# Performance work log

Hardware: AMD Instinct MI355X
Metric: run time of the kernel (lower is better)

## Reference

```python
import jax, jax.numpy as jnp
import numpy as np

B, N, D = 256, 100000, 512
A, C, K = 256, 100, 32
EPS = 1e-8  # torch cosine_similarity eps


def setup_inputs() -> dict:
    key = jax.random.key(0)
    ks = jax.random.split(key, 10)
    s = lambda fan_in: 1.0 / np.sqrt(fan_in)
    return {
        "query_feat": jax.random.normal(ks[0], (B, D), jnp.float32),
        "memory_keys": jax.random.normal(ks[1], (N, D), jnp.float32),
        # query_dense: Linear(D, A)
        "Wq": jax.random.uniform(ks[2], (D, A), jnp.float32, -s(D), s(D)),
        "bq": jax.random.uniform(ks[3], (A,), jnp.float32, -s(D), s(D)),
        # memory_dense: Linear(D, A)
        "Wm": jax.random.uniform(ks[4], (D, A), jnp.float32, -s(D), s(D)),
        "bm": jax.random.uniform(ks[5], (A,), jnp.float32, -s(D), s(D)),
        # attention_score_dense: Linear(A, 1)
        "Ws": jax.random.uniform(ks[6], (A, 1), jnp.float32, -s(A), s(A)),
        "bs": jax.random.uniform(ks[7], (1,), jnp.float32, -s(A), s(A)),
        # classification_layer: Linear(2*D, C)
        "Wc": jax.random.uniform(ks[8], (2 * D, C), jnp.float32, -s(2 * D), s(2 * D)),
        "bc": jax.random.uniform(ks[9], (C,), jnp.float32, -s(2 * D), s(2 * D)),
    }


def reference(query_feat, memory_keys, Wq, bq, Wm, bm, Ws, bs, Wc, bc):
    # query embedding (visual encoder output) + relu
    q = jax.nn.relu(query_feat)  # [B, D]
    # ---- knn_search: cosine similarity + topk + gather ----
    qn = jnp.linalg.norm(q, axis=-1)            # [B]
    kn = jnp.linalg.norm(memory_keys, axis=-1)  # [N]
    sim = (q @ memory_keys.T) / jnp.maximum(qn[:, None] * kn[None, :], EPS)  # [B, N]
    _, idx = jax.lax.top_k(sim, K)              # [B, K]
    knn = memory_keys[idx]                      # [B, K, D]
    # ---- MemoryAttentionModule ----
    # tanh(query_dense(q)[:,None,:] + memory_dense(knn)) -> score -> softmax over K
    h = jnp.tanh((q @ Wq + bq)[:, None, :] + knn @ Wm + bm)  # [B, K, A]
    scores = h @ Ws + bs                                      # [B, K, 1]
    w = jax.nn.softmax(scores, axis=1)                        # [B, K, 1]
    attended = jnp.sum(w * knn, axis=1)                       # [B, D]
    # ---- classification ----
    merged = jnp.concatenate([q, attended], axis=1)           # [B, 2D]
    return merged @ Wc + bc                                   # [B, C]
```

## Files before the change

kernel.cpp:

```cpp
#include <hip/hip_runtime.h>
#include <hip/hip_bf16.h>
#include <hip/hip_fp16.h>

#define BQ    256
#define NKEY  100000
#define DD    512
#define AD    256
#define CD    100
#define KSEL  32
#define KB    64
#define NB    1563
#define CPQ   (NB*12)

#define NPART 8
#define WTOP  12
#define NC2   (NPART*4*WTOP)
#define TLA   6

typedef __attribute__((ext_vector_type(8))) short  short8_t;
typedef __attribute__((ext_vector_type(8))) __bf16 bf16x8;
typedef __attribute__((ext_vector_type(4))) float  f32x4;

__device__ __forceinline__ unsigned short f2bf(float x) {
  unsigned int u = __float_as_uint(x);
  return (unsigned short)((u + 0x7FFFu + ((u >> 16) & 1u)) >> 16);
}
__device__ __forceinline__ unsigned short f2bf_n(float x) {
  __bf16 h = (__bf16)x;
  return __builtin_bit_cast(unsigned short, h);
}
__device__ __forceinline__ float bf2f(unsigned short h) {
  return __uint_as_float(((unsigned int)h) << 16);
}
__device__ __forceinline__ f32x4 mfma_bf16(short8_t a, short8_t b, f32x4 c) {
  return __builtin_amdgcn_mfma_f32_16x16x32_bf16(
      __builtin_bit_cast(bf16x8, a), __builtin_bit_cast(bf16x8, b), c, 0, 0, 0);
}
__device__ __forceinline__ float fast_tanh(float x) {
  x = fminf(fmaxf(x, -15.f), 15.f);
  float e = __expf(2.f * x);
  return (e - 1.f) * __builtin_amdgcn_rcpf(e + 1.f);
}
__device__ __forceinline__ void gload_lds16(const float* g, float* l) {
  __builtin_amdgcn_global_load_lds((const __attribute__((address_space(1))) void*)g,
                                   (__attribute__((address_space(3))) void*)l, 16, 0, 0);
}

template<int T>
__device__ __forceinline__ void topk_insert(float (&v)[T], int (&ix)[T], float val, int idx) {
  if (val <= v[T-1]) return;
  v[T-1] = val; ix[T-1] = idx;
  #pragma unroll
  for (int j = T-1; j > 0; --j) {
    bool sw = v[j] > v[j-1];
    float tv = sw ? v[j] : v[j-1];  float uv = sw ? v[j-1] : v[j];
    int   ti = sw ? ix[j] : ix[j-1]; int  ui = sw ? ix[j-1] : ix[j];
    v[j-1] = tv; v[j] = uv; ix[j-1] = ti; ix[j] = ui;
  }
}

__global__ __launch_bounds__(256) void k0_prep(const float* __restrict__ qfeat,
                                               float* __restrict__ qr,
                                               unsigned short* __restrict__ qf,
                                               float* __restrict__ qn) {
  int b = blockIdx.x, t = threadIdx.x;
  float s = 0.f;
  #pragma unroll
  for (int p = 0; p < 2; ++p) {
    int k = t + p*256;
    float v = qfeat[b*DD + k];
    v = v > 0.f ? v : 0.f;
    qr[b*DD + k] = v;
    qf[(((b>>4)*64 + (k>>3))*16 + (b&15))*8 + (k&7)] = f2bf(v);
    s += v*v;
  }
  __shared__ float red[4];
  #pragma unroll
  for (int st = 1; st < 64; st <<= 1) s += __shfl_xor(s, st, 64);
  if ((t & 63) == 0) red[t>>6] = s;
  __syncthreads();
  if (t == 0) qn[b] = sqrtf(red[0]+red[1]+red[2]+red[3]);
}

__global__ __launch_bounds__(256) void k0b_frag(const float* __restrict__ W,
                                                unsigned short* __restrict__ wf) {
  int i = blockIdx.x*256 + threadIdx.x;
  int d = i >> 8, a = i & 255;
  wf[(((a>>4)*64 + (d>>3))*16 + (a&15))*8 + (d&7)] = f2bf(W[i]);
}

__global__ __launch_bounds__(256) void k_qq(const float* __restrict__ Wq,
                                            const unsigned short* __restrict__ qf,
                                            const float* __restrict__ bq,
                                            const float* __restrict__ bm,
                                            float* __restrict__ qq) {
  __shared__ unsigned short wb[64*16*8];
  int bn = blockIdx.x & 15, rg = blockIdx.x >> 4;
  int t = threadIdx.x;
  int w = t >> 6, l = t & 63, g = l >> 4, c = l & 15;
  #pragma unroll
  for (int i = 0; i < 32; ++i) {
    int d = i*16 + (t>>4); int a = t & 15;
    wb[((d>>3)*16 + a)*8 + (d&7)] = f2bf(Wq[d*AD + bn*16 + a]);
  }
  __syncthreads();
  const short8_t* qf8 = (const short8_t*)qf;
  const short8_t* wb8 = (const short8_t*)wb;
  f32x4 acc = (f32x4){0.f,0.f,0.f,0.f};
  int M = rg*4 + w;
  for (int kt = 0; kt < 16; ++kt) {
    short8_t bfr = wb8[(kt*4 + g)*16 + c];
    short8_t afr = qf8[(M*64 + kt*4 + g)*16 + c];
    acc = mfma_bf16(afr, bfr, acc);
  }
  int col = bn*16 + c;
  float bias = bq[col] + bm[col];
  #pragma unroll
  for (int r = 0; r < 4; ++r)
    qq[(M*16 + g*4 + r)*AD + col] = acc[r] + bias;
}

__global__ __launch_bounds__(256) void k1_sim(const float* __restrict__ keys,
                                              const unsigned short* __restrict__ qf,
                                              unsigned int* __restrict__ cand) {
  __shared__ float At[3][64*64];
  __shared__ float invkn[64];

  int b = blockIdx.x, t = threadIdx.x;
  int kb0 = b*KB;
  int w = t >> 6, l = t & 63, g = l >> 4, c = l & 15;

  f32x4 acc[4][4];
  #pragma unroll
  for (int m = 0; m < 4; ++m)
    #pragma unroll
    for (int n = 0; n < 4; ++n) acc[m][n] = (f32x4){0.f,0.f,0.f,0.f};
  float ksq = 0.f;

  const short8_t* qf8 = (const short8_t*)qf;

  auto stage = [&](int buf, int k0) {
    #pragma unroll
    for (int i = 0; i < 4; ++i) {
      int gidx = i*256 + t;
      int r = gidx >> 4, gg = gidx & 15;
      int row = kb0 + r; row = row < NKEY ? row : NKEY-1;
      const float* src = keys + (size_t)row*DD + k0 + ((gg ^ (r & 7)) << 2);
      float* dst = &At[buf][0] + (i*256 + w*64)*4;
      gload_lds16(src, dst);
    }
  };

  short8_t Bcur[2][4];
  #pragma unroll
  for (int kt = 0; kt < 2; ++kt)
    #pragma unroll
    for (int n = 0; n < 4; ++n)
      Bcur[kt][n] = qf8[((w*4 + n)*64 + kt*4 + g)*16 + c];
  __builtin_amdgcn_sched_barrier(0);
  stage(0, 0);
  stage(1, 64);

  #pragma unroll
  for (int ks8 = 0; ks8 < 8; ++ks8) {
    if (ks8 < 7) asm volatile("s_waitcnt vmcnt(4)" ::: "memory");
    else         asm volatile("s_waitcnt vmcnt(0)" ::: "memory");
    __builtin_amdgcn_s_barrier();
    __builtin_amdgcn_sched_barrier(0);
    short8_t Bnxt[2][4];
    if (ks8 < 7) {
      #pragma unroll
      for (int kt = 0; kt < 2; ++kt)
        #pragma unroll
        for (int n = 0; n < 4; ++n)
          Bnxt[kt][n] = qf8[((w*4 + n)*64 + (ks8+1)*8 + kt*4 + g)*16 + c];
    }
    __builtin_amdgcn_sched_barrier(0);
    if (ks8 < 6) stage((ks8 + 2) % 3, (ks8 + 2)*64);
    __builtin_amdgcn_sched_barrier(0);
    int cur = ks8 % 3;
    int p = c & 7;
    #pragma unroll
    for (int kt = 0; kt < 2; ++kt) {
      int S = kt*8 + g*2;
      int g_lo = S ^ p, g_hi = (S + 1) ^ p;
      #pragma unroll
      for (int m = 0; m < 4; ++m) {
        const float* ab = &At[cur][0] + (m*16 + c)*64;
        float4 lo = *(const float4*)(ab + g_lo*4);
        float4 hi = *(const float4*)(ab + g_hi*4);
        if (m == w) {
          ksq += lo.x*lo.x + lo.y*lo.y + lo.z*lo.z + lo.w*lo.w
               + hi.x*hi.x + hi.y*hi.y + hi.z*hi.z + hi.w*hi.w;
        }
        short8_t af;
        af[0] = (short)f2bf_n(lo.x); af[1] = (short)f2bf_n(lo.y);
        af[2] = (short)f2bf_n(lo.z); af[3] = (short)f2bf_n(lo.w);
        af[4] = (short)f2bf_n(hi.x); af[5] = (short)f2bf_n(hi.y);
        af[6] = (short)f2bf_n(hi.z); af[7] = (short)f2bf_n(hi.w);
        #pragma unroll
        for (int n = 0; n < 4; ++n) acc[m][n] = mfma_bf16(af, Bcur[kt][n], acc[m][n]);
      }
    }
    if (ks8 < 7) {
      #pragma unroll
      for (int kt = 0; kt < 2; ++kt)
        #pragma unroll
        for (int n = 0; n < 4; ++n) Bcur[kt][n] = Bnxt[kt][n];
    }
  }

  {
    float s = ksq;
    s += __shfl_xor(s, 16, 64);
    s += __shfl_xor(s, 32, 64);
    if (l < 16) invkn[w*16 + l] = s > 0.f ? rsqrtf(s) : 0.f;
  }
  __syncthreads();

  float ikv[16];
  #pragma unroll
  for (int m = 0; m < 4; ++m)
    #pragma unroll
    for (int r = 0; r < 4; ++r) ikv[m*4 + r] = invkn[m*16 + g*4 + r];

  #pragma unroll
  for (int n = 0; n < 4; ++n) {
    float v1 = -3.0e38f, v2 = -3.0e38f, v3 = -3.0e38f;
    int   i1 = 0, i2 = 0, i3 = 0;
    #pragma unroll
    for (int m = 0; m < 4; ++m)
      #pragma unroll
      for (int r = 0; r < 4; ++r) {
        int lid = m*16 + g*4 + r;
        bool valid = (kb0 + lid) < NKEY;
        float v = valid ? acc[m][n][r] * ikv[m*4 + r] : -3.0e38f;
        bool gt1 = v > v1, gt2 = v > v2, gt3 = v > v3;
        v3 = gt2 ? v2 : (gt3 ? v : v3);  i3 = gt2 ? i2 : (gt3 ? lid : i3);
        v2 = gt1 ? v1 : (gt2 ? v : v2);  i2 = gt1 ? i1 : (gt2 ? lid : i2);
        v1 = gt1 ? v  : v1;              i1 = gt1 ? lid : i1;
      }
    int q = w*64 + n*16 + c;
    unsigned int base = ((unsigned int)q*NB + (unsigned int)b)*12u + (unsigned int)g*3u;
    cand[base + 0] = ((unsigned int)__half_as_ushort(__float2half(v1)) << 16) | (unsigned int)i1;
    cand[base + 1] = ((unsigned int)__half_as_ushort(__float2half(v2)) << 16) | (unsigned int)i2;
    cand[base + 2] = ((unsigned int)__half_as_ushort(__float2half(v3)) << 16) | (unsigned int)i3;
  }
}

__global__ __launch_bounds__(256) void k2a_reduce(const unsigned int* __restrict__ cand,
                                                  const float* __restrict__ qr,
                                                  const float* __restrict__ qn,
                                                  const float* __restrict__ keys,
                                                  float* __restrict__ wtopv,
                                                  int* __restrict__ wtopi) {
  int bid = blockIdx.x;
  int q = bid >> 3, p = bid & 7;
  int t = threadIdx.x, w = t >> 6, l = t & 63;
  const unsigned int* cq = cand + (size_t)q * CPQ;

  const int PER_PART = (CPQ + NPART - 1) / NPART;
  const int PER_WAVE = (PER_PART + 3) / 4;
  int pbase = p * PER_PART;
  int start = pbase + w * PER_WAVE;
  int end   = pbase + PER_PART;
  if (start + PER_WAVE < end) end = start + PER_WAVE;
  if (end > CPQ) end = CPQ;

  float v[TLA]; int ix[TLA];
  #pragma unroll
  for (int j = 0; j < TLA; ++j) { v[j] = -INFINITY; ix[j] = -1; }
  for (int i = start + l; i < end; i += 64) {
    unsigned int pk = cq[i];
    float val = __half2float(__ushort_as_half((unsigned short)(pk >> 16)));
    int bb = i / 12;
    int idx = (bb << 6) | (int)(pk & 63u);
    topk_insert<TLA>(v, ix, val, idx);
  }

  int idxs[WTOP];
  for (int it = 0; it < WTOP; ++it) {
    float bv = v[0]; int bx = ix[0]; int bl = l;
    #pragma unroll
    for (int sft = 1; sft < 64; sft <<= 1) {
      float ov = __shfl_xor(bv, sft, 64);
      int  oxx = __shfl_xor(bx, sft, 64);
      int  ol  = __shfl_xor(bl, sft, 64);
      bool take = (ov > bv) || (ov == bv && ol < bl);
      if (take) { bv = ov; bx = oxx; bl = ol; }
    }
    idxs[it] = bx;
    if (l == bl) {
      #pragma unroll
      for (int j = 0; j < TLA-1; ++j) { v[j] = v[j+1]; ix[j] = ix[j+1]; }
      v[TLA-1] = -INFINITY; ix[TLA-1] = -1;
    }
  }

  const float4* q4 = (const float4*)(qr + (size_t)q*DD + l*8);
  float4 qa0 = q4[0], qa1 = q4[1];
  float qnv = qn[q];
  int obase = (q * NPART + p) * 4 * WTOP + w * WTOP;

  int nidx = idxs[0];
  const float4* kr = (const float4*)(keys + (size_t)((nidx < 0 || nidx >= NKEY) ? 0 : nidx)*DD + l*8);
  float4 k0v = kr[0], k1v = kr[1];
  for (int j = 0; j < WTOP; ++j) {
    int curidx = idxs[j];
    bool bad = (curidx < 0) || (curidx >= NKEY);
    float4 c0 = k0v, c1 = k1v;
    if (j + 1 < WTOP) {
      nidx = idxs[j+1];
      kr = (const float4*)(keys + (size_t)((nidx < 0 || nidx >= NKEY) ? 0 : nidx)*DD + l*8);
      k0v = kr[0]; k1v = kr[1];
    }
    float dot = qa0.x*c0.x + qa0.y*c0.y + qa0.z*c0.z + qa0.w*c0.w
              + qa1.x*c1.x + qa1.y*c1.y + qa1.z*c1.z + qa1.w*c1.w;
    float ks  = c0.x*c0.x + c0.y*c0.y + c0.z*c0.z + c0.w*c0.w
              + c1.x*c1.x + c1.y*c1.y + c1.z*c1.z + c1.w*c1.w;
    #pragma unroll
    for (int sft = 1; sft < 64; sft <<= 1) {
      dot += __shfl_xor(dot, sft, 64);
      ks  += __shfl_xor(ks,  sft, 64);
    }
    if (l == 0) {
      float den = fmaxf(qnv * sqrtf(ks), 1e-8f);
      wtopv[obase + j] = bad ? -1e30f : dot/den;
      wtopi[obase + j] = bad ? 0 : curidx;
    }
  }
}

__global__ __launch_bounds__(256) void k23ab(const float* __restrict__ wtopv,
                                             const int* __restrict__ wtopi,
                                             const float* __restrict__ keys,
                                             const float* __restrict__ qq,
                                             const unsigned short* __restrict__ wmf,
                                             const float* __restrict__ Ws,
                                             const float* __restrict__ bsc,
                                             unsigned short* __restrict__ attf) {
  int q = blockIdx.x, t = threadIdx.x, w = t >> 6, l = t & 63, g = l >> 4, c = l & 15;
  __shared__ float simx[NC2];
  __shared__ int   sidx[NC2];
  __shared__ int   fl[KSEL];
  __shared__ float qqb[256];
  __shared__ float wsl[256];
  __shared__ unsigned short knnb[32*520];
  __shared__ float spart[4][32];
  __shared__ float wexp[32];

  qqb[t] = qq[q*AD + t];
  wsl[t] = Ws[t];
  for (int i = t; i < NC2; i += 256) {
    simx[i] = wtopv[q*NC2 + i];
    int idx = wtopi[q*NC2 + i];
    sidx[i] = (idx < 0 || idx >= NKEY) ? 0 : idx;
  }
  __syncthreads();

  if (w == 0) {
    float a[6]; int id[6];
    #pragma unroll
    for (int j = 0; j < 6; ++j) { a[j] = simx[j*64 + l]; id[j] = sidx[j*64 + l]; }
    for (int it = 0; it < KSEL; ++it) {
      float bv = a[0]; int bx = id[0]; int bslot = 0;
      #pragma unroll
      for (int j = 1; j < 6; ++j) {
        bool take = (a[j] > bv) || (a[j] == bv && id[j] < bx);
        bv = take ? a[j] : bv; bx = take ? id[j] : bx; bslot = take ? j : bslot;
      }
      int bl = l;
      #pragma unroll
      for (int sft = 1; sft < 64; sft <<= 1) {
        float ov = __shfl_xor(bv, sft, 64);
        int  oxx = __shfl_xor(bx, sft, 64);
        int  ol  = __shfl_xor(bl, sft, 64);
        bool take = (ov > bv) || (ov == bv && oxx < bx);
        if (take) { bv = ov; bx = oxx; bl = ol; }
      }
      if (l == 0) fl[it] = bx;
      if (l == bl) {
        #pragma unroll
        for (int j = 0; j < 6; ++j) if (j == bslot) a[j] = -INFINITY;
      }
    }
  }
  __syncthreads();

  #pragma unroll 4
  for (int rr = 0; rr < 32; rr += 2) {
    int r = rr + (t >> 7);
    int row = fl[r];
    int d4 = t & 127;
    float4 v = *(const float4*)(keys + (size_t)row*DD + d4*4);
    ushort4 h; h.x = f2bf_n(v.x); h.y = f2bf_n(v.y); h.z = f2bf_n(v.z); h.w = f2bf_n(v.w);
    *(ushort4*)&knnb[r*520 + d4*4] = h;
  }
  __syncthreads();

  f32x4 acc[2][4];
  #pragma unroll
  for (int m = 0; m < 2; ++m)
    #pragma unroll
    for (int n = 0; n < 4; ++n) acc[m][n] = (f32x4){0.f,0.f,0.f,0.f};
  const short8_t* wmf8 = (const short8_t*)wmf;
  for (int ks = 0; ks < 16; ++ks) {
    short8_t af[2], bf[4];
    #pragma unroll
    for (int m = 0; m < 2; ++m) af[m] = *(const short8_t*)&knnb[(m*16 + c)*520 + ks*32 + g*8];
    #pragma unroll
    for (int n = 0; n < 4; ++n) bf[n] = wmf8[((w*4 + n)*64 + ks*4 + g)*16 + c];
    #pragma unroll
    for (int m = 0; m < 2; ++m)
      #pragma unroll
      for (int n = 0; n < 4; ++n) acc[m][n] = mfma_bf16(af[m], bf[n], acc[m][n]);
  }

  float p[8] = {0.f,0.f,0.f,0.f,0.f,0.f,0.f,0.f};
  #pragma unroll
  for (int n = 0; n < 4; ++n) {
    int a = w*64 + n*16 + c;
    float qv = qqb[a], wv = wsl[a];
    #pragma unroll
    for (int m = 0; m < 2; ++m)
      #pragma unroll
      for (int r = 0; r < 4; ++r)
        p[m*4 + r] += fast_tanh(acc[m][n][r] + qv) * wv;
  }
  #pragma unroll
  for (int sft = 1; sft < 16; sft <<= 1)
    #pragma unroll
    for (int i = 0; i < 8; ++i) p[i] += __shfl_xor(p[i], sft, 64);
  if (c == 0) {
    #pragma unroll
    for (int m = 0; m < 2; ++m)
      #pragma unroll
      for (int r = 0; r < 4; ++r) spart[w][m*16 + g*4 + r] = p[m*4 + r];
  }
  __syncthreads();

  if (t < 32) {
    float s = spart[0][t] + spart[1][t] + spart[2][t] + spart[3][t] + bsc[0];
    float mx = s;
    #pragma unroll
    for (int sft = 1; sft < 32; sft <<= 1) mx = fmaxf(mx, __shfl_xor(mx, sft, 64));
    float e = __expf(s - mx);
    float su = e;
    #pragma unroll
    for (int sft = 1; sft < 32; sft <<= 1) su += __shfl_xor(su, sft, 64);
    wexp[t] = e / su;
  }
  __syncthreads();

  #pragma unroll
  for (int pth = 0; pth < 2; ++pth) {
    int d = t + pth*256;
    float s = 0.f;
    #pragma unroll
    for (int k = 0; k < 32; ++k) s += wexp[k] * bf2f(knnb[k*520 + d]);
    attf[(((q>>4)*64 + (d>>3))*16 + (q&15))*8 + (d&7)] = f2bf(s);
  }
}

__global__ __launch_bounds__(256) void k3b_cls(const float* __restrict__ Wc,
                                               const unsigned short* __restrict__ qf,
                                               const unsigned short* __restrict__ attf,
                                               const float* __restrict__ bc,
                                               float* __restrict__ out) {
  __shared__ unsigned short wb[128*16*8];
  int bn = blockIdx.x, t = threadIdx.x;
  int w = t >> 6, l = t & 63, g = l >> 4, c = l & 15;
  #pragma unroll
  for (int i = 0; i < 64; ++i) {
    int d = i*16 + (t>>4); int a = t & 15;
    int col = bn*16 + a;
    float vv = (col < CD) ? Wc[d*CD + col] : 0.f;
    wb[((d>>3)*16 + a)*8 + (d&7)] = f2bf(vv);
  }
  __syncthreads();
  const short8_t* qf8 = (const short8_t*)qf;
  const short8_t* af8 = (const short8_t*)attf;
  const short8_t* wb8 = (const short8_t*)wb;
  f32x4 acc[4];
  #pragma unroll
  for (int m = 0; m < 4; ++m) acc[m] = (f32x4){0.f,0.f,0.f,0.f};
  for (int kt = 0; kt < 32; ++kt) {
    short8_t bfr = wb8[(kt*4 + g)*16 + c];
    const short8_t* asrc = (kt < 16) ? qf8 : af8;
    int kbase = (kt < 16) ? (kt*4 + g) : ((kt-16)*4 + g);
    #pragma unroll
    for (int m = 0; m < 4; ++m) {
      short8_t afr = asrc[((w*4 + m)*64 + kbase)*16 + c];
      acc[m] = mfma_bf16(afr, bfr, acc[m]);
    }
  }
  int col = bn*16 + c;
  if (col < CD) {
    float bias = bc[col];
    #pragma unroll
    for (int m = 0; m < 4; ++m)
      #pragma unroll
      for (int r = 0; r < 4; ++r)
        out[(w*64 + m*16 + g*4 + r)*CD + col] = acc[m][r] + bias;
  }
}

extern "C" void kernel_launch(void* const* d_in, const int* in_sizes, int n_in,
                              void* d_out, int out_size, void* d_ws, size_t ws_size,
                              hipStream_t stream) {
  const float* qfeat = (const float*)d_in[0];
  const float* keys  = (const float*)d_in[1];
  const float* Wq    = (const float*)d_in[2];
  const float* bq    = (const float*)d_in[3];
  const float* Wm    = (const float*)d_in[4];
  const float* bm    = (const float*)d_in[5];
  const float* Ws    = (const float*)d_in[6];
  const float* bsc   = (const float*)d_in[7];
  const float* Wc    = (const float*)d_in[8];
  const float* bc    = (const float*)d_in[9];
  float* out = (float*)d_out;

  char* ws = (char*)d_ws;
  unsigned short* qf   = (unsigned short*)(ws + 0);
  float*          qr   = (float*)(ws + 262144);
  float*          qn   = (float*)(ws + 786432);
  unsigned short* wmf  = (unsigned short*)(ws + 787456);
  float*          qq   = (float*)(ws + 1049600);
  unsigned short* attf = (unsigned short*)(ws + 1311744);
  float*          wtopv= (float*)(ws + 1573888);
  int*            wtopi= (int*)(ws + 1967104);
  unsigned int*   cand = (unsigned int*)(ws + 2360320);

  k0_prep   <<<BQ,       256, 0, stream>>>(qfeat, qr, qf, qn);
  k0b_frag  <<<512,      256, 0, stream>>>(Wm, wmf);
  k_qq      <<<64,       256, 0, stream>>>(Wq, qf, bq, bm, qq);
  k1_sim    <<<NB,       256, 0, stream>>>(keys, qf, cand);
  k2a_reduce<<<BQ*NPART, 256, 0, stream>>>(cand, qr, qn, keys, wtopv, wtopi);
  k23ab     <<<BQ,       256, 0, stream>>>(wtopv, wtopi, keys, qq, wmf, Ws, bsc, attf);
  k3b_cls   <<<7,        256, 0, stream>>>(Wc, qf, attf, bc, out);
}
```

Measured before the change: 185.2 us.

## Convert key tiles to bf16 once in registers before LDS staging

Key tiles are no longer copied as fp32 into a triple-buffered LDS ring with direct global-to-LDS loads. Each thread now loads its slice into registers, computes the key norm partials, converts to bf16 once, and writes a single swizzled bf16 LDS tile. This removes the redundant fp32-to-bf16 conversions done by all four waves and shrinks LDS from 48KB to about 8KB, which could raise occupancy. The cost is a register-prefetch pipeline only one stage deep, with a full vmcnt(0) wait and two barriers per k-step, so global latency may be less hidden.

```diff
diff --git a/kernel.cpp b/kernel.cpp
--- a/kernel.cpp
+++ b/kernel.cpp
@@ -41,10 +41,6 @@
   float e = __expf(2.f * x);
   return (e - 1.f) * __builtin_amdgcn_rcpf(e + 1.f);
 }
-__device__ __forceinline__ void gload_lds16(const float* g, float* l) {
-  __builtin_amdgcn_global_load_lds((const __attribute__((address_space(1))) void*)g,
-                                   (__attribute__((address_space(3))) void*)l, 16, 0, 0);
-}
 
 template<int T>
 __device__ __forceinline__ void topk_insert(float (&v)[T], int (&ix)[T], float val, int idx) {
@@ -123,7 +119,7 @@
 __global__ __launch_bounds__(256) void k1_sim(const float* __restrict__ keys,
                                               const unsigned short* __restrict__ qf,
                                               unsigned int* __restrict__ cand) {
-  __shared__ float At[3][64*64];
+  __shared__ short8_t Abf8[64*8];
   __shared__ float invkn[64];
 
   int b = blockIdx.x, t = threadIdx.x;
@@ -135,21 +131,17 @@
   for (int m = 0; m < 4; ++m)
     #pragma unroll
     for (int n = 0; n < 4; ++n) acc[m][n] = (f32x4){0.f,0.f,0.f,0.f};
-  float ksq = 0.f;
 
   const short8_t* qf8 = (const short8_t*)qf;
 
-  auto stage = [&](int buf, int k0) {
-    #pragma unroll
-    for (int i = 0; i < 4; ++i) {
-      int gidx = i*256 + t;
-      int r = gidx >> 4, gg = gidx & 15;
-      int row = kb0 + r; row = row < NKEY ? row : NKEY-1;
-      const float* src = keys + (size_t)row*DD + k0 + ((gg ^ (r & 7)) << 2);
-      float* dst = &At[buf][0] + (i*256 + w*64)*4;
-      gload_lds16(src, dst);
-    }
-  };
+  int r1 = t >> 3, gb = t & 7;
+  int r2 = 32 + r1;
+  int swz = gb ^ (r1 & 7);
+  int row1 = kb0 + r1; row1 = row1 < NKEY ? row1 : NKEY-1;
+  int row2 = kb0 + r2; row2 = row2 < NKEY ? row2 : NKEY-1;
+  const float* src1 = keys + (size_t)row1*DD + gb*8;
+  const float* src2 = keys + (size_t)row2*DD + gb*8;
+  float ksq1 = 0.f, ksq2 = 0.f;
 
   short8_t Bcur[2][4];
   #pragma unroll
@@ -157,16 +149,30 @@
     #pragma unroll
     for (int n = 0; n < 4; ++n)
       Bcur[kt][n] = qf8[((w*4 + n)*64 + kt*4 + g)*16 + c];
-  __builtin_amdgcn_sched_barrier(0);
-  stage(0, 0);
-  stage(1, 64);
+  float4 a0 = *(const float4*)(src1);
+  float4 a1 = *(const float4*)(src1 + 4);
+  float4 b0 = *(const float4*)(src2);
+  float4 b1 = *(const float4*)(src2 + 4);
 
   #pragma unroll
   for (int ks8 = 0; ks8 < 8; ++ks8) {
-    if (ks8 < 7) asm volatile("s_waitcnt vmcnt(4)" ::: "memory");
-    else         asm volatile("s_waitcnt vmcnt(0)" ::: "memory");
+    asm volatile("s_waitcnt vmcnt(0)" ::: "memory");
+    ksq1 += a0.x*a0.x + a0.y*a0.y + a0.z*a0.z + a0.w*a0.w
+          + a1.x*a1.x + a1.y*a1.y + a1.z*a1.z + a1.w*a1.w;
+    ksq2 += b0.x*b0.x + b0.y*b0.y + b0.z*b0.z + b0.w*b0.w
+          + b1.x*b1.x + b1.y*b1.y + b1.z*b1.z + b1.w*b1.w;
+    short8_t w1, w2;
+    w1[0] = (short)f2bf_n(a0.x); w1[1] = (short)f2bf_n(a0.y);
+    w1[2] = (short)f2bf_n(a0.z); w1[3] = (short)f2bf_n(a0.w);
+    w1[4] = (short)f2bf_n(a1.x); w1[5] = (short)f2bf_n(a1.y);
+    w1[6] = (short)f2bf_n(a1.z); w1[7] = (short)f2bf_n(a1.w);
+    w2[0] = (short)f2bf_n(b0.x); w2[1] = (short)f2bf_n(b0.y);
+    w2[2] = (short)f2bf_n(b0.z); w2[3] = (short)f2bf_n(b0.w);
+    w2[4] = (short)f2bf_n(b1.x); w2[5] = (short)f2bf_n(b1.y);
+    w2[6] = (short)f2bf_n(b1.z); w2[7] = (short)f2bf_n(b1.w);
     __builtin_amdgcn_s_barrier();
-    __builtin_amdgcn_sched_barrier(0);
+    Abf8[r1*8 + swz] = w1;
+    Abf8[r2*8 + swz] = w2;
     short8_t Bnxt[2][4];
     if (ks8 < 7) {
       #pragma unroll
@@ -174,32 +180,22 @@
         #pragma unroll
         for (int n = 0; n < 4; ++n)
           Bnxt[kt][n] = qf8[((w*4 + n)*64 + (ks8+1)*8 + kt*4 + g)*16 + c];
-    }
+      a0 = *(const float4*)(src1 + (ks8+1)*64);
+      a1 = *(const float4*)(src1 + (ks8+1)*64 + 4);
+      b0 = *(const float4*)(src2 + (ks8+1)*64);
+      b1 = *(const float4*)(src2 + (ks8+1)*64 + 4);
+    }
+    asm volatile("s_waitcnt lgkmcnt(0)" ::: "memory");
+    __builtin_amdgcn_s_barrier();
     __builtin_amdgcn_sched_barrier(0);
-    if (ks8 < 6) stage((ks8 + 2) % 3, (ks8 + 2)*64);
-    __builtin_amdgcn_sched_barrier(0);
-    int cur = ks8 % 3;
     int p = c & 7;
     #pragma unroll
     for (int kt = 0; kt < 2; ++kt) {
-      int S = kt*8 + g*2;
-      int g_lo = S ^ p, g_hi = (S + 1) ^ p;
       #pragma unroll
       for (int m = 0; m < 4; ++m) {
-        const float* ab = &At[cur][0] + (m*16 + c)*64;
-        float4 lo = *(const float4*)(ab + g_lo*4);
-        float4 hi = *(const float4*)(ab + g_hi*4);
-        if (m == w) {
-          ksq += lo.x*lo.x + lo.y*lo.y + lo.z*lo.z + lo.w*lo.w
-               + hi.x*hi.x + hi.y*hi.y + hi.z*hi.z + hi.w*hi.w;
-        }
-        short8_t af;
-        af[0] = (short)f2bf_n(lo.x); af[1] = (short)f2bf_n(lo.y);
-        af[2] = (short)f2bf_n(lo.z); af[3] = (short)f2bf_n(lo.w);
-        af[4] = (short)f2bf_n(hi.x); af[5] = (short)f2bf_n(hi.y);
-        af[6] = (short)f2bf_n(hi.z); af[7] = (short)f2bf_n(hi.w);
+        short8_t A = Abf8[(m*16 + c)*8 + ((kt*4 + g) ^ p)];
         #pragma unroll
-        for (int n = 0; n < 4; ++n) acc[m][n] = mfma_bf16(af, Bcur[kt][n], acc[m][n]);
+        for (int n = 0; n < 4; ++n) acc[m][n] = mfma_bf16(A, Bcur[kt][n], acc[m][n]);
       }
     }
     if (ks8 < 7) {
@@ -210,11 +206,11 @@
     }
   }
 
-  {
-    float s = ksq;
-    s += __shfl_xor(s, 16, 64);
-    s += __shfl_xor(s, 32, 64);
-    if (l < 16) invkn[w*16 + l] = s > 0.f ? rsqrtf(s) : 0.f;
+  ksq1 += __shfl_xor(ksq1, 1, 64); ksq1 += __shfl_xor(ksq1, 2, 64); ksq1 += __shfl_xor(ksq1, 4, 64);
+  ksq2 += __shfl_xor(ksq2, 1, 64); ksq2 += __shfl_xor(ksq2, 2, 64); ksq2 += __shfl_xor(ksq2, 4, 64);
+  if ((t & 7) == 0) {
+    invkn[r1] = ksq1 > 0.f ? rsqrtf(ksq1) : 0.f;
+    invkn[r2] = ksq2 > 0.f ? rsqrtf(ksq2) : 0.f;
   }
   __syncthreads();
 
```

New measurement: 183.7 us. Within noise of the previous version (-0.8%).
